# Performance work log

Measured on AMD Instinct MI355X. Metric: run time of the kernel, lower is better.

## Reference

```python
import jax, jax.numpy as jnp
import numpy as np

L, B, D = 512, 64, 512  # seq_len, batch (hardcoded in module), in_size == hidden_size


def setup_inputs() -> dict:
    key = jax.random.key(0)
    ks = jax.random.split(key, 10)
    H = D
    s = 1.0 / np.sqrt(H)
    return {
        "v": jax.random.normal(ks[0], (L, B, D), dtype=jnp.float32),
        "h0": jax.random.normal(ks[1], (B, H), dtype=jnp.float32),   # self.h = randn(B,H)
        "V": jax.random.normal(ks[2], (B, H, 1), dtype=jnp.float32),  # self.V = randn(B,H,1)
        "Wp": jax.random.normal(ks[3], (H, D), dtype=jnp.float32) * s,
        "Wp_": jax.random.normal(ks[4], (H, D), dtype=jnp.float32) * s,
        "W_ih": jax.random.normal(ks[5], (3 * H, D), dtype=jnp.float32) * s,
        "W_hh": jax.random.normal(ks[6], (3 * H, H), dtype=jnp.float32) * s,
        "b_ih": jax.random.normal(ks[7], (3 * H,), dtype=jnp.float32) * s,
        "b_hh": jax.random.normal(ks[8], (3 * H,), dtype=jnp.float32) * s,
    }


def _gru_cell(x, h, W_ih, W_hh, b_ih, b_hh):
    # PyTorch GRUCell semantics
    gi = x @ W_ih.T + b_ih          # (B, 3H)
    gh = h @ W_hh.T + b_hh          # (B, 3H)
    i_r, i_z, i_n = jnp.split(gi, 3, axis=-1)
    h_r, h_z, h_n = jnp.split(gh, 3, axis=-1)
    r = jax.nn.sigmoid(i_r + h_r)
    z = jax.nn.sigmoid(i_z + h_z)
    n = jnp.tanh(i_n + r * h_n)
    return (1.0 - z) * n + z * h


def reference(v, h0, V, Wp, Wp_, W_ih, W_hh, b_ih, b_hh):
    # Precompute both projections once (original redundantly recomputes Wp_(v) per step)
    Wpv = jnp.einsum('lbd,hd->lbh', v, Wp)    # Wp(v[i]) for all i
    Wp_v = jnp.einsum('lbd,hd->lbh', v, Wp_)  # Wp_(v)
    Vb = V[:, :, 0]                            # (B, H)

    def step(h, wpv_i):
        x = jnp.tanh(wpv_i[None, :, :] + Wp_v)        # (L, B, H)
        s = jnp.einsum('lbh,bh->bl', x, Vb)            # scores over sequence
        a = jax.nn.softmax(s, axis=1)                  # (B, L)
        c = jnp.einsum('bl,lbd->bd', a, v)             # attended context
        h_new = _gru_cell(c, h, W_ih, W_hh, b_ih, b_hh)
        return h_new, h_new

    _, hs = jax.lax.scan(step, h0, Wpv)  # hs: (L, B, H)
    # dropout is identity in eval mode
    return hs
```

## Files before the change

### kernel.cpp

```cpp
#include <hip/hip_runtime.h>
#include <hip/hip_bf16.h>


typedef float f32x4 __attribute__((ext_vector_type(4)));
typedef short s16x8 __attribute__((ext_vector_type(8)));
typedef short s16x4 __attribute__((ext_vector_type(4)));
typedef unsigned int u32x2 __attribute__((ext_vector_type(2)));

static __device__ __forceinline__ float rcp_fast(float x) { return __builtin_amdgcn_rcpf(x); }
static __device__ __forceinline__ float tanh_fast(float x) {
    float e = __expf(2.0f * x);
    return 1.0f - 2.0f * rcp_fast(e + 1.0f);
}
static __device__ __forceinline__ float sigmoid_fast(float x) {
    return rcp_fast(1.0f + __expf(-x));
}
static __device__ __forceinline__ unsigned short f2bf(float x) {
    union { float f; unsigned u; } v; v.f = x;
    unsigned r = v.u + 0x7FFFu + ((v.u >> 16) & 1u);
    return (unsigned short)(r >> 16);
}
static __device__ __forceinline__ float bf2f(unsigned short b) {
    union { unsigned u; float f; } v; v.u = ((unsigned)b) << 16;
    return v.f;
}
static __device__ __forceinline__ s16x8 pack8(f32x4 a, f32x4 b) {
    s16x8 r;
    r[0] = (short)f2bf(a[0]); r[1] = (short)f2bf(a[1]);
    r[2] = (short)f2bf(a[2]); r[3] = (short)f2bf(a[3]);
    r[4] = (short)f2bf(b[0]); r[5] = (short)f2bf(b[1]);
    r[6] = (short)f2bf(b[2]); r[7] = (short)f2bf(b[3]);
    return r;
}
static __device__ __forceinline__ void split8(f32x4 a, f32x4 b, s16x8* hi, s16x8* lo) {
    s16x8 h, l;
#pragma unroll
    for (int e = 0; e < 4; e++) {
        unsigned short hh = f2bf(a[e]); h[e] = (short)hh;
        l[e] = (short)f2bf(a[e] - bf2f(hh));
    }
#pragma unroll
    for (int e = 0; e < 4; e++) {
        unsigned short hh = f2bf(b[e]); h[4 + e] = (short)hh;
        l[4 + e] = (short)f2bf(b[e] - bf2f(hh));
    }
    *hi = h; *lo = l;
}
static __device__ __forceinline__ f32x4 mfma16(s16x8 a, s16x8 b, f32x4 c) {
    return __builtin_amdgcn_mfma_f32_16x16x32_bf16(a, b, c, 0, 0, 0);
}
static __device__ __forceinline__ unsigned ld_agent(const unsigned* p) {
    return __hip_atomic_load(p, __ATOMIC_RELAXED, __HIP_MEMORY_SCOPE_AGENT);
}
static __device__ __forceinline__ void add_agent(unsigned* p, unsigned v) {
    __hip_atomic_fetch_add(p, v, __ATOMIC_RELAXED, __HIP_MEMORY_SCOPE_AGENT);
}
static __device__ __forceinline__ void vm_drain() {
    asm volatile("s_waitcnt vmcnt(0)" ::: "memory");
}

__global__ __launch_bounds__(256, 2)
void pq_k(const float* __restrict__ v, const float* __restrict__ Wp,
          const float* __restrict__ Wp_, float* __restrict__ Ep,
          float* __restrict__ Eq)
{
    const int bm = blockIdx.x, bn = blockIdx.y;
    const int tid = threadIdx.x;
    const int w = tid >> 6, lane = tid & 63;
    const int l15 = lane & 15, l4 = lane >> 4;

    __shared__ unsigned short Al[128 * 72 * 2];
    __shared__ unsigned short Wl[128 * 72 * 2];
    const int LOFS = 128 * 72;

    f32x4 accP[4][4], accQ[4][4];
#pragma unroll
    for (int i = 0; i < 4; i++)
#pragma unroll
        for (int j = 0; j < 4; j++) {
            accP[i][j] = (f32x4){0.f, 0.f, 0.f, 0.f};
            accQ[i][j] = (f32x4){0.f, 0.f, 0.f, 0.f};
        }

    const int srow = tid >> 1, shalf = tid & 1;
    const float* Asrc  = v   + (size_t)(bm * 128 + srow) * 512 + shalf * 32;
    const float* W1src = Wp  + (size_t)(bn * 128 + srow) * 512 + shalf * 32;
    const float* W2src = Wp_ + (size_t)(bn * 128 + srow) * 512 + shalf * 32;
    unsigned short* Adst = Al + srow * 72 + shalf * 32;
    unsigned short* Wdst = Wl + srow * 72 + shalf * 32;

    for (int k0 = 0; k0 < 512; k0 += 64) {
        __syncthreads();
#pragma unroll
        for (int j = 0; j < 4; j++) {
            f32x4 x = *(const f32x4*)(Asrc + k0 + j * 8);
            f32x4 y = *(const f32x4*)(Asrc + k0 + j * 8 + 4);
            s16x8 hi, lo; split8(x, y, &hi, &lo);
            *(s16x8*)(Adst + j * 8) = hi;
            *(s16x8*)(Adst + LOFS + j * 8) = lo;
        }
#pragma unroll
        for (int j = 0; j < 4; j++) {
            f32x4 x = *(const f32x4*)(W1src + k0 + j * 8);
            f32x4 y = *(const f32x4*)(W1src + k0 + j * 8 + 4);
            s16x8 hi, lo; split8(x, y, &hi, &lo);
            *(s16x8*)(Wdst + j * 8) = hi;
            *(s16x8*)(Wdst + LOFS + j * 8) = lo;
        }
        __syncthreads();

#pragma unroll
        for (int kt = 0; kt < 2; kt++) {
            s16x8 afh[4], afl[4], bfh[4], bfl[4];
#pragma unroll
            for (int mb = 0; mb < 4; mb++) {
                afh[mb] = *(const s16x8*)(Al + ((w & 1) * 64 + mb * 16 + l15) * 72 + kt * 32 + l4 * 8);
                afl[mb] = *(const s16x8*)(Al + LOFS + ((w & 1) * 64 + mb * 16 + l15) * 72 + kt * 32 + l4 * 8);
            }
#pragma unroll
            for (int nb = 0; nb < 4; nb++) {
                bfh[nb] = *(const s16x8*)(Wl + ((w >> 1) * 64 + nb * 16 + l15) * 72 + kt * 32 + l4 * 8);
                bfl[nb] = *(const s16x8*)(Wl + LOFS + ((w >> 1) * 64 + nb * 16 + l15) * 72 + kt * 32 + l4 * 8);
            }
#pragma unroll
            for (int mb = 0; mb < 4; mb++)
#pragma unroll
                for (int nb = 0; nb < 4; nb++) {
                    accP[mb][nb] = mfma16(afh[mb], bfh[nb], accP[mb][nb]);
                    accP[mb][nb] = mfma16(afh[mb], bfl[nb], accP[mb][nb]);
                    accP[mb][nb] = mfma16(afl[mb], bfh[nb], accP[mb][nb]);
                }
        }

        __syncthreads();
#pragma unroll
        for (int j = 0; j < 4; j++) {
            f32x4 x = *(const f32x4*)(W2src + k0 + j * 8);
            f32x4 y = *(const f32x4*)(W2src + k0 + j * 8 + 4);
            s16x8 hi, lo; split8(x, y, &hi, &lo);
            *(s16x8*)(Wdst + j * 8) = hi;
            *(s16x8*)(Wdst + LOFS + j * 8) = lo;
        }
        __syncthreads();

#pragma unroll
        for (int kt = 0; kt < 2; kt++) {
            s16x8 afh[4], afl[4], bfh[4], bfl[4];
#pragma unroll
            for (int mb = 0; mb < 4; mb++) {
                afh[mb] = *(const s16x8*)(Al + ((w & 1) * 64 + mb * 16 + l15) * 72 + kt * 32 + l4 * 8);
                afl[mb] = *(const s16x8*)(Al + LOFS + ((w & 1) * 64 + mb * 16 + l15) * 72 + kt * 32 + l4 * 8);
            }
#pragma unroll
            for (int nb = 0; nb < 4; nb++) {
                bfh[nb] = *(const s16x8*)(Wl + ((w >> 1) * 64 + nb * 16 + l15) * 72 + kt * 32 + l4 * 8);
                bfl[nb] = *(const s16x8*)(Wl + LOFS + ((w >> 1) * 64 + nb * 16 + l15) * 72 + kt * 32 + l4 * 8);
            }
#pragma unroll
            for (int mb = 0; mb < 4; mb++)
#pragma unroll
                for (int nb = 0; nb < 4; nb++) {
                    accQ[mb][nb] = mfma16(afh[mb], bfh[nb], accQ[mb][nb]);
                    accQ[mb][nb] = mfma16(afh[mb], bfl[nb], accQ[mb][nb]);
                    accQ[mb][nb] = mfma16(afl[mb], bfh[nb], accQ[mb][nb]);
                }
        }
    }

    const int m0 = bm * 128 + (w & 1) * 64;
    const int n0 = bn * 128 + (w >> 1) * 64;
#pragma unroll
    for (int nb = 0; nb < 4; nb++) {
        const int n = n0 + nb * 16 + l15;
#pragma unroll
        for (int mb = 0; mb < 4; mb++) {
#pragma unroll
            for (int i = 0; i < 4; i++) {
                const int m = m0 + mb * 16 + l4 * 4 + i;
                Ep[(size_t)m * 512 + n] = __expf(2.0f * accP[mb][nb][i]);
                Eq[(size_t)m * 512 + n] = __expf(2.0f * accQ[mb][nb][i]);
            }
        }
    }
}

__global__ __launch_bounds__(256, 2)
void gi_k(const unsigned short* __restrict__ Ap, const float* __restrict__ Wp,
          const float* __restrict__ bias, unsigned short* __restrict__ outp, int N)
{
    const int bm = blockIdx.x, bn = blockIdx.y;
    const int tid = threadIdx.x;
    const int w = tid >> 6, lane = tid & 63;
    const int l15 = lane & 15, l4 = lane >> 4;

    __shared__ unsigned short Al[128 * 72];
    __shared__ unsigned short Wl[128 * 72];

    f32x4 acc[4][4];
#pragma unroll
    for (int i = 0; i < 4; i++)
#pragma unroll
        for (int j = 0; j < 4; j++) acc[i][j] = (f32x4){0.f, 0.f, 0.f, 0.f};

    const int srow = tid >> 1, shalf = tid & 1;
    const unsigned short* Asrcb = Ap + (size_t)(bm * 128 + srow) * 512 + shalf * 32;
    const float* Wsrc = Wp + (size_t)(bn * 128 + srow) * 512 + shalf * 32;
    unsigned short* Adst = Al + srow * 72 + shalf * 32;
    unsigned short* Wdst = Wl + srow * 72 + shalf * 32;

    for (int k0 = 0; k0 < 512; k0 += 64) {
        __syncthreads();
#pragma unroll
        for (int j = 0; j < 4; j++)
            *(s16x8*)(Adst + j * 8) = *(const s16x8*)(Asrcb + k0 + j * 8);
#pragma unroll
        for (int j = 0; j < 4; j++) {
            f32x4 x = *(const f32x4*)(Wsrc + k0 + j * 8);
            f32x4 y = *(const f32x4*)(Wsrc + k0 + j * 8 + 4);
            *(s16x8*)(Wdst + j * 8) = pack8(x, y);
        }
        __syncthreads();

#pragma unroll
        for (int kt = 0; kt < 2; kt++) {
            s16x8 afh[4], bfh[4];
#pragma unroll
            for (int mb = 0; mb < 4; mb++)
                afh[mb] = *(const s16x8*)(Al + ((w & 1) * 64 + mb * 16 + l15) * 72 + kt * 32 + l4 * 8);
#pragma unroll
            for (int nb = 0; nb < 4; nb++)
                bfh[nb] = *(const s16x8*)(Wl + ((w >> 1) * 64 + nb * 16 + l15) * 72 + kt * 32 + l4 * 8);
#pragma unroll
            for (int mb = 0; mb < 4; mb++)
#pragma unroll
                for (int nb = 0; nb < 4; nb++)
                    acc[mb][nb] = mfma16(afh[mb], bfh[nb], acc[mb][nb]);
        }
    }

    const int m0 = bm * 128 + (w & 1) * 64;
    const int n0 = bn * 128 + (w >> 1) * 64;
#pragma unroll
    for (int nb = 0; nb < 4; nb++) {
        const int n = n0 + nb * 16 + l15;
        const float bv = bias[n];
#pragma unroll
        for (int mb = 0; mb < 4; mb++) {
#pragma unroll
            for (int i = 0; i < 4; i++) {
                const int m = m0 + mb * 16 + l4 * 4 + i;
                outp[(size_t)m * N + n] = f2bf(acc[mb][nb][i] + bv);
            }
        }
    }
}

__global__ __launch_bounds__(512, 4)
void att_k(const float* __restrict__ Ept, const float* __restrict__ Eqt,
           const float* __restrict__ Vv, const float* __restrict__ vin,
           unsigned short* __restrict__ cbuf)
{
    const int tblk = blockIdx.x, b = blockIdx.y;
    const int tid = threadIdx.x;
    const int w = tid >> 6, lane = tid & 63;
    const int t_in = lane >> 5, sl = lane & 31;
    const int t_loc = w * 2 + t_in;
    const int tg = tblk * 16 + t_loc;

    __shared__ float sbuf[16][513];
    __shared__ float qst[8][640];
    __shared__ float zinv[16];

    float Ep[16], Vb2[16];
    float VbS = 0.0f;
    {
        const float* pp = Ept + ((size_t)tg * 64 + b) * 512 + sl * 16;
        const float* vb = Vv + (size_t)b * 512 + sl * 16;
#pragma unroll
        for (int j = 0; j < 4; j++) {
            f32x4 x = *(const f32x4*)(pp + j * 4);
            f32x4 y = *(const f32x4*)(vb + j * 4);
#pragma unroll
            for (int e = 0; e < 4; e++) {
                Ep[j * 4 + e] = x[e];
                Vb2[j * 4 + e] = 2.0f * y[e];
                VbS += y[e];
            }
        }
    }

    for (int l0 = 0; l0 < 512; l0 += 8) {
        __syncthreads();
        {
            const int row = tid >> 6;
            const int cb = (tid & 63) * 8;
            const float* src = Eqt + ((size_t)(l0 + row) * 64 + b) * 512 + cb;
            const int f0 = cb + 4 * (cb >> 4);
            *(f32x4*)(&qst[row][f0])     = *(const f32x4*)(src);
            *(f32x4*)(&qst[row][f0 + 4]) = *(const f32x4*)(src + 4);
        }
        __syncthreads();
        for (int l = 0; l < 8; l++) {
            const float* qrow = &qst[l][sl * 20];
            float a0 = VbS, a1 = 0.f;
#pragma unroll
            for (int j = 0; j < 4; j++) {
                f32x4 q = *(const f32x4*)(qrow + j * 4);
                float d0 = fmaf(Ep[4 * j + 0], q[0], 1.0f);
                float d1 = fmaf(Ep[4 * j + 1], q[1], 1.0f);
                float d2 = fmaf(Ep[4 * j + 2], q[2], 1.0f);
                float d3 = fmaf(Ep[4 * j + 3], q[3], 1.0f);
                float m01 = d0 * d1;
                float m23 = d2 * d3;
                float n01 = Vb2[4 * j + 0] * d1;
                n01 = fmaf(Vb2[4 * j + 1], d0, n01);
                float n23 = Vb2[4 * j + 2] * d3;
                n23 = fmaf(Vb2[4 * j + 3], d2, n23);
                a0 = fmaf(-n01, rcp_fast(m01), a0);
                a1 = fmaf(-n23, rcp_fast(m23), a1);
            }
            float accp = a0 + a1;
#pragma unroll
            for (int m = 1; m < 32; m <<= 1) accp += __shfl_xor(accp, m, 64);
            if (sl == 0) sbuf[t_loc][l0 + l] = accp;
        }
    }
    __syncthreads();

    {
        const int tr = tid >> 5;
        const int i = tid & 31;
        float m = -1e30f;
        for (int l = i; l < 512; l += 32) m = fmaxf(m, sbuf[tr][l]);
#pragma unroll
        for (int mm = 1; mm < 32; mm <<= 1) m = fmaxf(m, __shfl_xor(m, mm, 64));
        float z = 0.0f;
        for (int l = i; l < 512; l += 32) {
            float e = __expf(sbuf[tr][l] - m);
            sbuf[tr][l] = e;
            z += e;
        }
#pragma unroll
        for (int mm = 1; mm < 32; mm <<= 1) z += __shfl_xor(z, mm, 64);
        if (i == 0) zinv[tr] = rcp_fast(z);
    }
    __syncthreads();

    float ca[16];
#pragma unroll
    for (int j = 0; j < 16; j++) ca[j] = 0.0f;

    for (int l0 = 0; l0 < 512; l0 += 8) {
        __syncthreads();
        {
            const int row = tid >> 6;
            const int cb = (tid & 63) * 8;
            const float* src = vin + ((size_t)(l0 + row) * 64 + b) * 512 + cb;
            const int f0 = cb + 4 * (cb >> 4);
            *(f32x4*)(&qst[row][f0])     = *(const f32x4*)(src);
            *(f32x4*)(&qst[row][f0 + 4]) = *(const f32x4*)(src + 4);
        }
        __syncthreads();
        for (int l = 0; l < 8; l++) {
            const float a = sbuf[t_loc][l0 + l];
            const float* vrow = &qst[l][sl * 20];
#pragma unroll
            for (int j = 0; j < 4; j++) {
                f32x4 x = *(const f32x4*)(vrow + j * 4);
                ca[4 * j + 0] = fmaf(a, x[0], ca[4 * j + 0]);
                ca[4 * j + 1] = fmaf(a, x[1], ca[4 * j + 1]);
                ca[4 * j + 2] = fmaf(a, x[2], ca[4 * j + 2]);
                ca[4 * j + 3] = fmaf(a, x[3], ca[4 * j + 3]);
            }
        }
    }
    const float zi = zinv[t_loc];
    unsigned short* co = cbuf + ((size_t)tg * 64 + b) * 512 + sl * 16;
#pragma unroll
    for (int j = 0; j < 4; j++) {
        s16x4 o;
        o[0] = (short)f2bf(ca[4 * j + 0] * zi);
        o[1] = (short)f2bf(ca[4 * j + 1] * zi);
        o[2] = (short)f2bf(ca[4 * j + 2] * zi);
        o[3] = (short)f2bf(ca[4 * j + 3] * zi);
        *(s16x4*)(co + j * 4) = o;
    }
}

__global__ __launch_bounds__(256, 1)
void rec_k(const unsigned short* __restrict__ Gi,
           const float* __restrict__ Whh, const float* __restrict__ bhh,
           const float* __restrict__ h0,
           unsigned int* __restrict__ hb32,
           unsigned int* __restrict__ bar,
           float* __restrict__ hs)
{
    const int tid = threadIdx.x;
    const int g = blockIdx.x >> 3;
    const int sub = blockIdx.x & 7;
    const int w = tid >> 6;
    const int lane = tid & 63;
    const int l15 = lane & 15, l4 = lane >> 4;
    const int b  = g * 8 + (l15 & 7);
    const int jb = sub * 64 + w * 16;
    const int jrow = l4 * 4;
    const bool writer = (l15 < 8);

    s16x8 wf[3][16];
#pragma unroll
    for (int gg = 0; gg < 3; gg++) {
        const float* wr = Whh + (size_t)(gg * 512 + jb + l15) * 512 + l4 * 8;
#pragma unroll
        for (int c = 0; c < 16; c++) {
            f32x4 x = *(const f32x4*)(wr + c * 32);
            f32x4 y = *(const f32x4*)(wr + c * 32 + 4);
            wf[gg][c] = pack8(x, y);
        }
    }

    float bh_r[4], bh_z[4], bh_n[4];
#pragma unroll
    for (int i = 0; i < 4; i++) {
        bh_r[i] = bhh[jb + jrow + i];
        bh_z[i] = bhh[512 + jb + jrow + i];
        bh_n[i] = bhh[1024 + jb + jrow + i];
    }
    float hp[4];
#pragma unroll
    for (int i = 0; i < 4; i++) hp[i] = h0[(size_t)b * 512 + jb + jrow + i];

    unsigned* barA = bar + g * 512;

    s16x4 g0, g1, g2;
    {
        const unsigned short* gp = Gi + (size_t)b * 1536 + jb + jrow;
        g0 = *(const s16x4*)(gp);
        g1 = *(const s16x4*)(gp + 512);
        g2 = *(const s16x4*)(gp + 1024);
    }

#define LDH(i, lit) asm volatile("global_load_dwordx4 %0, %1, off offset:" lit " sc1" \
                                 : "=v"(hfrag2[i]) : "v"(src) : "memory");

    for (int t = 0; t < 512; t++) {
        s16x8 hfrag[16];
        if (t == 0) {
            const float* hr = h0 + (size_t)b * 512 + l4 * 8;
#pragma unroll
            for (int c = 0; c < 16; c++) {
                f32x4 x = *(const f32x4*)(hr + c * 32);
                f32x4 y = *(const f32x4*)(hr + c * 32 + 4);
                hfrag[c] = pack8(x, y);
            }
        } else {
            const unsigned int* src = hb32 + (t & 1) * 16384 + b * 256 + l4 * 4;
            s16x8 hfrag2[16];
            LDH(0, "0")   LDH(1, "64")  LDH(2, "128")  LDH(3, "192")
            LDH(4, "256") LDH(5, "320") LDH(6, "384")  LDH(7, "448")
            LDH(8, "512") LDH(9, "576") LDH(10, "640") LDH(11, "704")
            LDH(12, "768") LDH(13, "832") LDH(14, "896") LDH(15, "960")
            vm_drain();
            __builtin_amdgcn_sched_barrier(0);
#pragma unroll
            for (int c = 0; c < 16; c++) hfrag[c] = hfrag2[c];
        }

        f32x4 acc0 = {0.f, 0.f, 0.f, 0.f};
        f32x4 acc1 = {0.f, 0.f, 0.f, 0.f};
        f32x4 acc2 = {0.f, 0.f, 0.f, 0.f};
#pragma unroll
        for (int c = 0; c < 16; c++) {
            acc0 = mfma16(wf[0][c], hfrag[c], acc0);
            acc1 = mfma16(wf[1][c], hfrag[c], acc1);
            acc2 = mfma16(wf[2][c], hfrag[c], acc2);
        }

#pragma unroll
        for (int i = 0; i < 4; i++) {
            float rr = sigmoid_fast(bf2f((unsigned short)g0[i]) + acc0[i] + bh_r[i]);
            float zz = sigmoid_fast(bf2f((unsigned short)g1[i]) + acc1[i] + bh_z[i]);
            float nn = tanh_fast(bf2f((unsigned short)g2[i]) + rr * (acc2[i] + bh_n[i]));
            hp[i] = fmaf(zz, hp[i] - nn, nn);
        }

        float* hso = hs + ((size_t)t * 64 + b) * 512 + jb + jrow;
        f32x4 hv = {hp[0], hp[1], hp[2], hp[3]};

        if (t < 511) {
            if (writer) {
                u32x2 pp;
                pp[0] = (unsigned)f2bf(hp[0]) | ((unsigned)f2bf(hp[1]) << 16);
                pp[1] = (unsigned)f2bf(hp[2]) | ((unsigned)f2bf(hp[3]) << 16);
                unsigned int* dst = hb32 + ((t + 1) & 1) * 16384 + b * 256 + ((jb + jrow) >> 1);
                asm volatile("global_store_dwordx2 %0, %1, off sc1"
                             :: "v"(dst), "v"(pp) : "memory");
            }
            vm_drain();
            __syncthreads();
            if (tid == 0) add_agent(barA + t, 1u);

            if (writer) *(f32x4*)hso = hv;
            s16x4 n0, n1, n2;
            {
                const unsigned short* gp = Gi + ((size_t)(t + 1) * 64 + b) * 1536 + jb + jrow;
                n0 = *(const s16x4*)(gp);
                n1 = *(const s16x4*)(gp + 512);
                n2 = *(const s16x4*)(gp + 1024);
            }

            for (;;) {
                unsigned vb = ld_agent(barA + t);
                if (vb >= 8u) break;
                __builtin_amdgcn_s_sleep(1);
            }
            g0 = n0; g1 = n1; g2 = n2;
        } else {
            if (writer) *(f32x4*)hso = hv;
        }
    }
#undef LDH
}

extern "C" void kernel_launch(void* const* d_in, const int* in_sizes, int n_in,
                              void* d_out, int out_size, void* d_ws, size_t ws_size,
                              hipStream_t stream)
{
    (void)in_sizes; (void)n_in; (void)out_size; (void)ws_size;
    const float* v   = (const float*)d_in[0];
    const float* h0  = (const float*)d_in[1];
    const float* Vv  = (const float*)d_in[2];
    const float* Wp  = (const float*)d_in[3];
    const float* Wp_ = (const float*)d_in[4];
    const float* Wih = (const float*)d_in[5];
    const float* Whh = (const float*)d_in[6];
    const float* bih = (const float*)d_in[7];
    const float* bhh = (const float*)d_in[8];
    float* hs = (float*)d_out;

    char* ws = (char*)d_ws;
    float* Ep = (float*)(ws);
    float* Eq = (float*)(ws + 67108864ULL);
    unsigned short* cb  = (unsigned short*)(ws + 134217728ULL);
    unsigned short* Gi  = (unsigned short*)(ws);
    unsigned int*   hb32 = (unsigned int*)(ws + 167772160ULL);
    unsigned int*   bar  = (unsigned int*)(ws + 167772160ULL + 131072ULL);

    hipMemsetAsync(bar, 0, 4096 * sizeof(unsigned int), stream);

    pq_k<<<dim3(256, 4), 256, 0, stream>>>(v, Wp, Wp_, Ep, Eq);

    att_k<<<dim3(32, 64), 512, 0, stream>>>(Ep, Eq, Vv, v, cb);

    gi_k<<<dim3(256, 12), 256, 0, stream>>>(cb, Wih, bih, Gi, 1536);

    rec_k<<<dim3(64), 256, 0, stream>>>(Gi, Whh, bhh, h0, hb32, bar, hs);
}
```

Measured before the change: 3.848 ms.

## Split attention context into softmax kernel plus bf16 MFMA batched GEMM

The attention kernel no longer computes the weighted context with scalar FMAs over v. It now writes normalized softmax weights as bf16 to a new buffer, and a separate batched GEMM kernel (ac_k) computes per-batch A(512x512) x v(512x512) with MFMA, transposing and packing v to bf16 in shared memory. This moves roughly 8.6 GFLOP of FP32 vector work onto matrix cores. In exchange it adds a 32MB intermediate write and read, one extra launch, and bf16 rounding of the attention weights and v.

```diff
diff --git a/kernel.cpp b/kernel.cpp
--- a/kernel.cpp
+++ b/kernel.cpp
@@ -184,81 +184,9 @@
     }
 }
 
-__global__ __launch_bounds__(256, 2)
-void gi_k(const unsigned short* __restrict__ Ap, const float* __restrict__ Wp,
-          const float* __restrict__ bias, unsigned short* __restrict__ outp, int N)
-{
-    const int bm = blockIdx.x, bn = blockIdx.y;
-    const int tid = threadIdx.x;
-    const int w = tid >> 6, lane = tid & 63;
-    const int l15 = lane & 15, l4 = lane >> 4;
-
-    __shared__ unsigned short Al[128 * 72];
-    __shared__ unsigned short Wl[128 * 72];
-
-    f32x4 acc[4][4];
-#pragma unroll
-    for (int i = 0; i < 4; i++)
-#pragma unroll
-        for (int j = 0; j < 4; j++) acc[i][j] = (f32x4){0.f, 0.f, 0.f, 0.f};
-
-    const int srow = tid >> 1, shalf = tid & 1;
-    const unsigned short* Asrcb = Ap + (size_t)(bm * 128 + srow) * 512 + shalf * 32;
-    const float* Wsrc = Wp + (size_t)(bn * 128 + srow) * 512 + shalf * 32;
-    unsigned short* Adst = Al + srow * 72 + shalf * 32;
-    unsigned short* Wdst = Wl + srow * 72 + shalf * 32;
-
-    for (int k0 = 0; k0 < 512; k0 += 64) {
-        __syncthreads();
-#pragma unroll
-        for (int j = 0; j < 4; j++)
-            *(s16x8*)(Adst + j * 8) = *(const s16x8*)(Asrcb + k0 + j * 8);
-#pragma unroll
-        for (int j = 0; j < 4; j++) {
-            f32x4 x = *(const f32x4*)(Wsrc + k0 + j * 8);
-            f32x4 y = *(const f32x4*)(Wsrc + k0 + j * 8 + 4);
-            *(s16x8*)(Wdst + j * 8) = pack8(x, y);
-        }
-        __syncthreads();
-
-#pragma unroll
-        for (int kt = 0; kt < 2; kt++) {
-            s16x8 afh[4], bfh[4];
-#pragma unroll
-            for (int mb = 0; mb < 4; mb++)
-                afh[mb] = *(const s16x8*)(Al + ((w & 1) * 64 + mb * 16 + l15) * 72 + kt * 32 + l4 * 8);
-#pragma unroll
-            for (int nb = 0; nb < 4; nb++)
-                bfh[nb] = *(const s16x8*)(Wl + ((w >> 1) * 64 + nb * 16 + l15) * 72 + kt * 32 + l4 * 8);
-#pragma unroll
-            for (int mb = 0; mb < 4; mb++)
-#pragma unroll
-                for (int nb = 0; nb < 4; nb++)
-                    acc[mb][nb] = mfma16(afh[mb], bfh[nb], acc[mb][nb]);
-        }
-    }
-
-    const int m0 = bm * 128 + (w & 1) * 64;
-    const int n0 = bn * 128 + (w >> 1) * 64;
-#pragma unroll
-    for (int nb = 0; nb < 4; nb++) {
-        const int n = n0 + nb * 16 + l15;
-        const float bv = bias[n];
-#pragma unroll
-        for (int mb = 0; mb < 4; mb++) {
-#pragma unroll
-            for (int i = 0; i < 4; i++) {
-                const int m = m0 + mb * 16 + l4 * 4 + i;
-                outp[(size_t)m * N + n] = f2bf(acc[mb][nb][i] + bv);
-            }
-        }
-    }
-}
-
 __global__ __launch_bounds__(512, 4)
-void att_k(const float* __restrict__ Ept, const float* __restrict__ Eqt,
-           const float* __restrict__ Vv, const float* __restrict__ vin,
-           unsigned short* __restrict__ cbuf)
+void att_s(const float* __restrict__ Ept, const float* __restrict__ Eqt,
+           const float* __restrict__ Vv, unsigned short* __restrict__ abuf)
 {
     const int tblk = blockIdx.x, b = blockIdx.y;
     const int tid = threadIdx.x;
@@ -346,44 +274,175 @@
     }
     __syncthreads();
 
-    float ca[16];
-#pragma unroll
-    for (int j = 0; j < 16; j++) ca[j] = 0.0f;
-
-    for (int l0 = 0; l0 < 512; l0 += 8) {
-        __syncthreads();
+    {
+        const int tr = tid >> 5;
+        const int i = tid & 31;
+        const float zi = zinv[tr];
+        const int tg2 = tblk * 16 + tr;
+        unsigned short* dst = abuf + ((size_t)b * 512 + tg2) * 512 + i * 16;
+        s16x8 o0, o1;
+#pragma unroll
+        for (int e = 0; e < 8; e++) o0[e] = (short)f2bf(sbuf[tr][i * 16 + e] * zi);
+#pragma unroll
+        for (int e = 0; e < 8; e++) o1[e] = (short)f2bf(sbuf[tr][i * 16 + 8 + e] * zi);
+        *(s16x8*)(dst)     = o0;
+        *(s16x8*)(dst + 8) = o1;
+    }
+}
+
+__global__ __launch_bounds__(256, 2)
+void ac_k(const unsigned short* __restrict__ abuf,
+          const float* __restrict__ vin,
+          unsigned short* __restrict__ cbuf)
+{
+    const int bt = blockIdx.x, bd = blockIdx.y, b = blockIdx.z;
+    const int tid = threadIdx.x;
+    const int w = tid >> 6, lane = tid & 63;
+    const int l15 = lane & 15, l4 = lane >> 4;
+
+    __shared__ unsigned short Al[128 * 72];
+    __shared__ unsigned short Wt[128 * 72];
+
+    f32x4 acc[4][4];
+#pragma unroll
+    for (int i = 0; i < 4; i++)
+#pragma unroll
+        for (int j = 0; j < 4; j++) acc[i][j] = (f32x4){0.f, 0.f, 0.f, 0.f};
+
+    const int srow = tid >> 1, shalf = tid & 1;
+    const unsigned short* Asrc = abuf + ((size_t)b * 512 + bt * 128 + srow) * 512 + shalf * 32;
+    unsigned short* Adst = Al + srow * 72 + shalf * 32;
+
+    const int lpair = tid & 31;
+    const int dgrp  = tid >> 5;
+
+    for (int k0 = 0; k0 < 512; k0 += 64) {
+        __syncthreads();
+#pragma unroll
+        for (int j = 0; j < 4; j++)
+            *(s16x8*)(Adst + j * 8) = *(const s16x8*)(Asrc + k0 + j * 8);
         {
-            const int row = tid >> 6;
-            const int cb = (tid & 63) * 8;
-            const float* src = vin + ((size_t)(l0 + row) * 64 + b) * 512 + cb;
-            const int f0 = cb + 4 * (cb >> 4);
-            *(f32x4*)(&qst[row][f0])     = *(const f32x4*)(src);
-            *(f32x4*)(&qst[row][f0 + 4]) = *(const f32x4*)(src + 4);
-        }
-        __syncthreads();
-        for (int l = 0; l < 8; l++) {
-            const float a = sbuf[t_loc][l0 + l];
-            const float* vrow = &qst[l][sl * 20];
+            const float* r0 = vin + ((size_t)(k0 + 2 * lpair) * 64 + b) * 512 + bd * 128 + dgrp * 16;
+            const float* r1 = r0 + 64 * 512;
+            f32x4 x0[4], x1[4];
 #pragma unroll
             for (int j = 0; j < 4; j++) {
-                f32x4 x = *(const f32x4*)(vrow + j * 4);
-                ca[4 * j + 0] = fmaf(a, x[0], ca[4 * j + 0]);
-                ca[4 * j + 1] = fmaf(a, x[1], ca[4 * j + 1]);
-                ca[4 * j + 2] = fmaf(a, x[2], ca[4 * j + 2]);
-                ca[4 * j + 3] = fmaf(a, x[3], ca[4 * j + 3]);
-            }
-        }
-    }
-    const float zi = zinv[t_loc];
-    unsigned short* co = cbuf + ((size_t)tg * 64 + b) * 512 + sl * 16;
-#pragma unroll
-    for (int j = 0; j < 4; j++) {
-        s16x4 o;
-        o[0] = (short)f2bf(ca[4 * j + 0] * zi);
-        o[1] = (short)f2bf(ca[4 * j + 1] * zi);
-        o[2] = (short)f2bf(ca[4 * j + 2] * zi);
-        o[3] = (short)f2bf(ca[4 * j + 3] * zi);
-        *(s16x4*)(co + j * 4) = o;
+                x0[j] = *(const f32x4*)(r0 + j * 4);
+                x1[j] = *(const f32x4*)(r1 + j * 4);
+            }
+            unsigned* wt32 = (unsigned*)Wt;
+#pragma unroll
+            for (int j = 0; j < 4; j++)
+#pragma unroll
+                for (int e = 0; e < 4; e++) {
+                    const int d = dgrp * 16 + j * 4 + e;
+                    wt32[d * 36 + lpair] =
+                        (unsigned)f2bf(x0[j][e]) | ((unsigned)f2bf(x1[j][e]) << 16);
+                }
+        }
+        __syncthreads();
+
+#pragma unroll
+        for (int kt = 0; kt < 2; kt++) {
+            s16x8 afh[4], bfh[4];
+#pragma unroll
+            for (int mb = 0; mb < 4; mb++)
+                afh[mb] = *(const s16x8*)(Al + ((w & 1) * 64 + mb * 16 + l15) * 72 + kt * 32 + l4 * 8);
+#pragma unroll
+            for (int nb = 0; nb < 4; nb++)
+                bfh[nb] = *(const s16x8*)(Wt + ((w >> 1) * 64 + nb * 16 + l15) * 72 + kt * 32 + l4 * 8);
+#pragma unroll
+            for (int mb = 0; mb < 4; mb++)
+#pragma unroll
+                for (int nb = 0; nb < 4; nb++)
+                    acc[mb][nb] = mfma16(afh[mb], bfh[nb], acc[mb][nb]);
+        }
+    }
+
+    const int t0 = bt * 128 + (w & 1) * 64;
+    const int d0 = bd * 128 + (w >> 1) * 64;
+#pragma unroll
+    for (int nb = 0; nb < 4; nb++) {
+        const int d = d0 + nb * 16 + l15;
+#pragma unroll
+        for (int mb = 0; mb < 4; mb++) {
+#pragma unroll
+            for (int i = 0; i < 4; i++) {
+                const int t = t0 + mb * 16 + l4 * 4 + i;
+                cbuf[((size_t)t * 64 + b) * 512 + d] = f2bf(acc[mb][nb][i]);
+            }
+        }
+    }
+}
+
+__global__ __launch_bounds__(256, 2)
+void gi_k(const unsigned short* __restrict__ Ap, const float* __restrict__ Wp,
+          const float* __restrict__ bias, unsigned short* __restrict__ outp, int N)
+{
+    const int bm = blockIdx.x, bn = blockIdx.y;
+    const int tid = threadIdx.x;
+    const int w = tid >> 6, lane = tid & 63;
+    const int l15 = lane & 15, l4 = lane >> 4;
+
+    __shared__ unsigned short Al[128 * 72];
+    __shared__ unsigned short Wl[128 * 72];
+
+    f32x4 acc[4][4];
+#pragma unroll
+    for (int i = 0; i < 4; i++)
+#pragma unroll
+        for (int j = 0; j < 4; j++) acc[i][j] = (f32x4){0.f, 0.f, 0.f, 0.f};
+
+    const int srow = tid >> 1, shalf = tid & 1;
+    const unsigned short* Asrcb = Ap + (size_t)(bm * 128 + srow) * 512 + shalf * 32;
+    const float* Wsrc = Wp + (size_t)(bn * 128 + srow) * 512 + shalf * 32;
+    unsigned short* Adst = Al + srow * 72 + shalf * 32;
+    unsigned short* Wdst = Wl + srow * 72 + shalf * 32;
+
+    for (int k0 = 0; k0 < 512; k0 += 64) {
+        __syncthreads();
+#pragma unroll
+        for (int j = 0; j < 4; j++)
+            *(s16x8*)(Adst + j * 8) = *(const s16x8*)(Asrcb + k0 + j * 8);
+#pragma unroll
+        for (int j = 0; j < 4; j++) {
+            f32x4 x = *(const f32x4*)(Wsrc + k0 + j * 8);
+            f32x4 y = *(const f32x4*)(Wsrc + k0 + j * 8 + 4);
+            *(s16x8*)(Wdst + j * 8) = pack8(x, y);
+        }
+        __syncthreads();
+
+#pragma unroll
+        for (int kt = 0; kt < 2; kt++) {
+            s16x8 afh[4], bfh[4];
+#pragma unroll
+            for (int mb = 0; mb < 4; mb++)
+                afh[mb] = *(const s16x8*)(Al + ((w & 1) * 64 + mb * 16 + l15) * 72 + kt * 32 + l4 * 8);
+#pragma unroll
+            for (int nb = 0; nb < 4; nb++)
+                bfh[nb] = *(const s16x8*)(Wl + ((w >> 1) * 64 + nb * 16 + l15) * 72 + kt * 32 + l4 * 8);
+#pragma unroll
+            for (int mb = 0; mb < 4; mb++)
+#pragma unroll
+                for (int nb = 0; nb < 4; nb++)
+                    acc[mb][nb] = mfma16(afh[mb], bfh[nb], acc[mb][nb]);
+        }
+    }
+
+    const int m0 = bm * 128 + (w & 1) * 64;
+    const int n0 = bn * 128 + (w >> 1) * 64;
+#pragma unroll
+    for (int nb = 0; nb < 4; nb++) {
+        const int n = n0 + nb * 16 + l15;
+        const float bv = bias[n];
+#pragma unroll
+        for (int mb = 0; mb < 4; mb++) {
+#pragma unroll
+            for (int i = 0; i < 4; i++) {
+                const int m = m0 + mb * 16 + l4 * 4 + i;
+                outp[(size_t)m * N + n] = f2bf(acc[mb][nb][i] + bv);
+            }
+        }
     }
 }
 
@@ -540,16 +599,19 @@
     char* ws = (char*)d_ws;
     float* Ep = (float*)(ws);
     float* Eq = (float*)(ws + 67108864ULL);
-    unsigned short* cb  = (unsigned short*)(ws + 134217728ULL);
-    unsigned short* Gi  = (unsigned short*)(ws);
-    unsigned int*   hb32 = (unsigned int*)(ws + 167772160ULL);
-    unsigned int*   bar  = (unsigned int*)(ws + 167772160ULL + 131072ULL);
+    unsigned short* abuf = (unsigned short*)(ws + 134217728ULL);
+    unsigned short* cb   = (unsigned short*)(ws + 167772160ULL);
+    unsigned short* Gi   = (unsigned short*)(ws);
+    unsigned int*   hb32 = (unsigned int*)(ws + 201326592ULL);
+    unsigned int*   bar  = (unsigned int*)(ws + 201326592ULL + 131072ULL);
 
     hipMemsetAsync(bar, 0, 4096 * sizeof(unsigned int), stream);
 
     pq_k<<<dim3(256, 4), 256, 0, stream>>>(v, Wp, Wp_, Ep, Eq);
 
-    att_k<<<dim3(32, 64), 512, 0, stream>>>(Ep, Eq, Vv, v, cb);
+    att_s<<<dim3(32, 64), 512, 0, stream>>>(Ep, Eq, Vv, abuf);
+
+    ac_k<<<dim3(4, 4, 64), 256, 0, stream>>>(abuf, v, cb);
 
     gi_k<<<dim3(256, 12), 256, 0, stream>>>(cb, Wih, bih, Gi, 1536);
 
```

After: 3.512 ms. -8.7%, faster.
